# Performance work log

Hardware: AMD Instinct MI355X
Metric: run time of the kernel (lower is better)

Reference implementation:

```python
import jax, jax.numpy as jnp
import numpy as np

N = 100000
D = 64
H = 4 * D  # 256
E = 1000000


def setup_inputs() -> dict:
    key = jax.random.key(0)
    ks = jax.random.split(key, 9)
    return {
        "loc_feat": jax.random.normal(ks[0], (N, D), dtype=jnp.float32),
        "geo_src": jax.random.randint(ks[1], (E,), 0, N),
        "geo_dst": jax.random.randint(ks[2], (E,), 0, N),
        "trans_src": jax.random.randint(ks[3], (E,), 0, N),
        "trans_dst": jax.random.randint(ks[4], (E,), 0, N),
        "trans_w": jax.random.uniform(ks[5], (E,), dtype=jnp.float32),
        "W1": jax.random.normal(ks[6], (D, H), dtype=jnp.float32) * (1.0 / np.sqrt(D)),
        "b1": jax.random.normal(ks[7], (H,), dtype=jnp.float32) * 0.01,
        "W2": jax.random.normal(ks[8], (H, 1), dtype=jnp.float32) * (1.0 / np.sqrt(H)),
    }


def reference(loc_feat, geo_src, geo_dst, trans_src, trans_dst, trans_w, W1, b1, W2):
    n = loc_feat.shape[0]
    # etype 'geo': copy_u + mean  -> segment mean of src features at dst
    geo_sum = jax.ops.segment_sum(loc_feat[geo_src], geo_dst, num_segments=n)
    cnt = jax.ops.segment_sum(jnp.ones(geo_src.shape[0], loc_feat.dtype), geo_dst, num_segments=n)
    geo = jnp.where(cnt[:, None] > 0, geo_sum / jnp.maximum(cnt, 1.0)[:, None], 0.0)
    # etype 'trans': u_mul_e + sum -> weighted segment sum
    trans = jax.ops.segment_sum(loc_feat[trans_src] * trans_w[:, None], trans_dst, num_segments=n)
    # semantic attention fuse over the two relation views
    z = jnp.stack([geo, trans], axis=1)          # [N, 2, D]
    h = jnp.tanh(jnp.einsum('nkd,dh->nkh', z, W1) + b1)  # [N, 2, H]
    w = jnp.einsum('nkh,ho->nko', h, W2).mean(0)  # [2, 1] (mean over nodes)
    beta = jax.nn.softmax(w, axis=0)              # [2, 1]
    return (beta[None, :, :] * z).sum(1)          # [N, D]
```

## Files before the change

### kernel.cpp

```cpp
#include <hip/hip_runtime.h>
#include <hip/hip_bf16.h>

#define N_NODES 100000
#define DIM 64
#define HID 256
#define E_EDGES 1000000
#define TWO_N (2 * N_NODES)
#define MLP_ROWBLOCKS (TWO_N / 64)

#define TILE 60
#define NBINS 1667
#define CAP 800
#define EPB 4096
#define FILL_BLOCKS 245

#define NCH 8
#define KEYS (TILE * NCH)

#define PACKF_BLOCKS 782
#define PACKW1_BLOCKS 32
#define PREP_BLOCKS (2 * FILL_BLOCKS + PACKF_BLOCKS + PACKW1_BLOCKS)

typedef short short8 __attribute__((ext_vector_type(8)));
typedef float f32x4 __attribute__((ext_vector_type(4)));
typedef unsigned short us4 __attribute__((ext_vector_type(4)));
typedef unsigned short us8 __attribute__((ext_vector_type(8)));

__device__ __forceinline__ float tanh_fast(float x) {
    x = fminf(fmaxf(x, -15.0f), 15.0f);
    float e = __expf(2.0f * x);
    return (e - 1.0f) / (e + 1.0f);
}

__device__ __forceinline__ unsigned short f2bf(float x) {
    unsigned u = __float_as_uint(x);
    u = u + 0x7FFFu + ((u >> 16) & 1u);
    return (unsigned short)(u >> 16);
}

__device__ __forceinline__ float bf2f(unsigned short u) {
    return __uint_as_float(((unsigned)u) << 16);
}

__global__ void __launch_bounds__(512) prep_kernel(
        const int* __restrict__ gs, const int* __restrict__ gd,
        const int* __restrict__ ts, const int* __restrict__ td,
        const float* __restrict__ tw,
        int* __restrict__ gcount,
        int* __restrict__ gbin, int2* __restrict__ tbin,
        const float* __restrict__ feat, unsigned short* __restrict__ fb,
        const float* __restrict__ W1, unsigned short* __restrict__ W1p) {
    __shared__ int   hist[NBINS];
    __shared__ int   adjS[NBINS];
    __shared__ int   curS[NBINS];
    __shared__ int   pS[EPB];
    __shared__ float w2S[EPB];
    __shared__ unsigned short binS[EPB];
    __shared__ int   wsumS[8];
    __shared__ int   wpreS[8];

    int t = threadIdx.x;
    int blk = blockIdx.x;

    if (blk >= 2 * FILL_BLOCKS) {
        int pb = blk - 2 * FILL_BLOCKS;
        if (pb < PACKF_BLOCKS) {
            #pragma unroll
            for (int j = 0; j < 4; ++j) {
                int i = pb * 2048 + j * 512 + t;
                if (i < N_NODES * DIM / 4) {
                    float4 v = ((const float4*)feat)[i];
                    us4 o;
                    o[0] = f2bf(v.x); o[1] = f2bf(v.y); o[2] = f2bf(v.z); o[3] = f2bf(v.w);
                    ((us4*)fb)[i] = o;
                }
            }
        } else {
            int i = (pb - PACKF_BLOCKS) * 512 + t;
            int j = i & 7;
            int r = i >> 3;
            int nidx = r & 15; r >>= 4;
            int q = r & 3; r >>= 2;
            int khalf = r & 1;
            int n = r >> 1;
            int k = 32 * khalf + 8 * q + j;
            int c = 16 * n + nidx;
            W1p[i] = f2bf(W1[k * HID + c]);
        }
        return;
    }

    int lane = t & 63, wv = t >> 6;
    int rel = (blk >= FILL_BLOCKS) ? 1 : 0;
    int e0 = (rel ? blk - FILL_BLOCKS : blk) * EPB;
    const int* dstp = rel ? td : gd;
    const int* srcp = rel ? ts : gs;

    for (int i = t; i < NBINS; i += 512) hist[i] = 0;
    __syncthreads();

    int d_[8], s_[8];
    float w_[8];
    #pragma unroll
    for (int j = 0; j < 2; ++j) {
        int idx = e0 + j * 2048 + 4 * t;
        if (idx + 3 < E_EDGES) {
            int4 dv = *(const int4*)&dstp[idx];
            int4 sv = *(const int4*)&srcp[idx];
            d_[4*j+0] = dv.x; d_[4*j+1] = dv.y; d_[4*j+2] = dv.z; d_[4*j+3] = dv.w;
            s_[4*j+0] = sv.x; s_[4*j+1] = sv.y; s_[4*j+2] = sv.z; s_[4*j+3] = sv.w;
            if (rel) {
                float4 wvv = *(const float4*)&tw[idx];
                w_[4*j+0] = wvv.x; w_[4*j+1] = wvv.y; w_[4*j+2] = wvv.z; w_[4*j+3] = wvv.w;
            }
        } else {
            #pragma unroll
            for (int i2 = 0; i2 < 4; ++i2) {
                bool ok = (idx + i2 < E_EDGES);
                d_[4*j+i2] = ok ? dstp[idx + i2] : -1;
                s_[4*j+i2] = ok ? srcp[idx + i2] : 0;
                w_[4*j+i2] = (ok && rel) ? tw[idx + i2] : 0.0f;
            }
        }
    }
    #pragma unroll
    for (int i = 0; i < 8; ++i)
        if (d_[i] >= 0) atomicAdd(&hist[d_[i] / TILE], 1);
    __syncthreads();

    int carry = 0;
    for (int cb = 0; cb < NBINS; cb += 512) {
        int i = cb + t;
        int c = (i < NBINS) ? hist[i] : 0;
        int v = c;
        #pragma unroll
        for (int off = 1; off < 64; off <<= 1) {
            int u = __shfl_up(v, off);
            if (lane >= off) v += u;
        }
        if (lane == 63) wsumS[wv] = v;
        __syncthreads();
        if (t == 0) {
            int s = 0;
            #pragma unroll
            for (int w = 0; w < 8; ++w) { s += wsumS[w]; wpreS[w] = s; }
        }
        __syncthreads();
        int woff = (wv == 0) ? 0 : wpreS[wv - 1];
        if (i < NBINS) {
            int lb = carry + woff + v - c;
            curS[i] = lb;
            int gb = (c > 0) ? (i * CAP + atomicAdd(&gcount[rel * NBINS + i], c)) : 0;
            adjS[i] = gb - lb;
        }
        carry += wpreS[7];
        __syncthreads();
    }
    __syncthreads();

    #pragma unroll
    for (int i = 0; i < 8; ++i) {
        int d = d_[i];
        if (d < 0) continue;
        int bin = d / TILE;
        int pos = atomicAdd(&curS[bin], 1);
        pS[pos] = s_[i] | ((d - bin * TILE) << 20);
        binS[pos] = (unsigned short)bin;
        if (rel) w2S[pos] = w_[i];
    }
    __syncthreads();

    int nV = min(EPB, E_EDGES - e0);
    if (!rel) {
        for (int i = t; i < nV; i += 512) {
            int b = binS[i];
            int gi = adjS[b] + i;
            if (gi < (b + 1) * CAP)
                gbin[gi] = pS[i];
        }
    } else {
        for (int i = t; i < nV; i += 512) {
            int b = binS[i];
            int gi = adjS[b] + i;
            if (gi < (b + 1) * CAP)
                tbin[gi] = make_int2(pS[i], __float_as_int(w2S[i]));
        }
    }
}

__global__ void __launch_bounds__(256) aggregate_kernel(
        const unsigned short* __restrict__ featb,
        const int* __restrict__ gbin, const int2* __restrict__ tbin,
        const int* __restrict__ gcount,
        unsigned short* __restrict__ zb) {
    __shared__ int   srcS[CAP];
    __shared__ float wS[CAP];
    __shared__ int   histK[KEYS];
    __shared__ int   keyBase[KEYS];
    __shared__ int   keyCur[KEYS];
    __shared__ int   nodeB[TILE];
    __shared__ int   nodeD[TILE];
    __shared__ int   wsA[4];
    __shared__ int   wpA[4];

    int b = blockIdx.x;
    int rel = (b >= NBINS) ? 1 : 0;
    int bin = rel ? b - NBINS : b;
    int node0 = bin * TILE;
    int nNodes = min(TILE, N_NODES - node0);
    int t = threadIdx.x, lane = t & 63, wave = t >> 6;
    int oct = lane >> 3;
    int co = (lane & 7) * 8;

    int nE = gcount[b];
    if (nE > CAP) nE = CAP;

    for (int i = t; i < KEYS; i += 256) histK[i] = 0;
    __syncthreads();

    if (!rel) {
        const int* bp = gbin + (size_t)bin * CAP;
        for (int i = t; i < nE; i += 256) {
            int p = bp[i];
            int key = ((p >> 20) << 3) | ((p & 0xFFFFF) >> 14);
            atomicAdd(&histK[key], 1);
        }
    } else {
        const int2* bp = tbin + (size_t)bin * CAP;
        for (int i = t; i < nE; i += 256) {
            int p = bp[i].x;
            int key = ((p >> 20) << 3) | ((p & 0xFFFFF) >> 14);
            atomicAdd(&histK[key], 1);
        }
    }
    __syncthreads();

    int carry = 0;
    for (int cb = 0; cb < KEYS; cb += 256) {
        int i = cb + t;
        int c = (i < KEYS) ? histK[i] : 0;
        int v = c;
        #pragma unroll
        for (int off = 1; off < 64; off <<= 1) {
            int u = __shfl_up(v, off);
            if (lane >= off) v += u;
        }
        if (lane == 63) wsA[wave] = v;
        __syncthreads();
        if (t == 0) {
            int s = 0;
            #pragma unroll
            for (int w = 0; w < 4; ++w) { s += wsA[w]; wpA[w] = s; }
        }
        __syncthreads();
        int woff = (wave == 0) ? 0 : wpA[wave - 1];
        if (i < KEYS) {
            int lb = carry + woff + v - c;
            keyBase[i] = lb;
            keyCur[i] = lb;
        }
        carry += wpA[3];
        __syncthreads();
    }
    if (t < TILE) {
        int nb = keyBase[t * NCH];
        int nx = (t == TILE - 1) ? nE : keyBase[(t + 1) * NCH];
        nodeB[t] = nb;
        nodeD[t] = nx - nb;
    }
    __syncthreads();

    if (!rel) {
        const int* bp = gbin + (size_t)bin * CAP;
        for (int i = t; i < nE; i += 256) {
            int p = bp[i];
            int key = ((p >> 20) << 3) | ((p & 0xFFFFF) >> 14);
            int pos = atomicAdd(&keyCur[key], 1);
            srcS[pos] = p & 0xFFFFF;
        }
    } else {
        const int2* bp = tbin + (size_t)bin * CAP;
        for (int i = t; i < nE; i += 256) {
            int2 p = bp[i];
            int key = ((p.x >> 20) << 3) | ((p.x & 0xFFFFF) >> 14);
            int pos = atomicAdd(&keyCur[key], 1);
            srcS[pos] = p.x & 0xFFFFF;
            wS[pos] = __int_as_float(p.y);
        }
    }
    __syncthreads();

    for (int nl0 = wave * 8; nl0 < nNodes; nl0 += 32) {
        int nl = nl0 + oct;
        bool act = (nl < nNodes);
        int deg = act ? nodeD[nl] : 0;
        int base = act ? nodeB[nl] : 0;
        float a[8] = {0.f, 0.f, 0.f, 0.f, 0.f, 0.f, 0.f, 0.f};
        if (!rel) {
            int k = 0;
            for (; k + 3 < deg; k += 4) {
                int s0 = srcS[base + k],     s1 = srcS[base + k + 1];
                int s2 = srcS[base + k + 2], s3 = srcS[base + k + 3];
                us8 r0 = *(const us8*)&featb[(size_t)s0 * DIM + co];
                us8 r1 = *(const us8*)&featb[(size_t)s1 * DIM + co];
                us8 r2 = *(const us8*)&featb[(size_t)s2 * DIM + co];
                us8 r3 = *(const us8*)&featb[(size_t)s3 * DIM + co];
                #pragma unroll
                for (int j = 0; j < 8; ++j)
                    a[j] += (bf2f(r0[j]) + bf2f(r1[j])) + (bf2f(r2[j]) + bf2f(r3[j]));
            }
            for (; k < deg; ++k) {
                int s = srcS[base + k];
                us8 r = *(const us8*)&featb[(size_t)s * DIM + co];
                #pragma unroll
                for (int j = 0; j < 8; ++j) a[j] += bf2f(r[j]);
            }
        } else {
            int k = 0;
            for (; k + 3 < deg; k += 4) {
                int s0 = srcS[base + k],     s1 = srcS[base + k + 1];
                int s2 = srcS[base + k + 2], s3 = srcS[base + k + 3];
                float w0 = wS[base + k],     w1 = wS[base + k + 1];
                float w2 = wS[base + k + 2], w3 = wS[base + k + 3];
                us8 r0 = *(const us8*)&featb[(size_t)s0 * DIM + co];
                us8 r1 = *(const us8*)&featb[(size_t)s1 * DIM + co];
                us8 r2 = *(const us8*)&featb[(size_t)s2 * DIM + co];
                us8 r3 = *(const us8*)&featb[(size_t)s3 * DIM + co];
                #pragma unroll
                for (int j = 0; j < 8; ++j)
                    a[j] += (bf2f(r0[j]) * w0 + bf2f(r1[j]) * w1)
                          + (bf2f(r2[j]) * w2 + bf2f(r3[j]) * w3);
            }
            for (; k < deg; ++k) {
                int s = srcS[base + k];
                float w = wS[base + k];
                us8 r = *(const us8*)&featb[(size_t)s * DIM + co];
                #pragma unroll
                for (int j = 0; j < 8; ++j) a[j] += bf2f(r[j]) * w;
            }
        }
        if (act) {
            float sc = rel ? 1.0f : 1.0f / fmaxf((float)deg, 1.0f);
            us8 o;
            #pragma unroll
            for (int j = 0; j < 8; ++j) o[j] = f2bf(a[j] * sc);
            size_t row = (size_t)(rel ? N_NODES + node0 + nl : node0 + nl);
            *(us8*)&zb[row * DIM + co] = o;
        }
    }
}

__global__ void __launch_bounds__(256) mlp_mfma_kernel(
        const unsigned short* __restrict__ zb,
        const unsigned short* __restrict__ W1p,
        const float* __restrict__ bias1, const float* __restrict__ W2,
        float* __restrict__ partials) {
    __shared__ float wred[4][2];
    int t = threadIdx.x, lane = t & 63, wave = t >> 6;
    int m = lane & 15, q = lane >> 4;
    int base = blockIdx.x * 64 + wave * 16;
    int R = base + m;

    const unsigned short* rowp = zb + (size_t)R * DIM;
    short8 a0 = *(const short8*)(rowp + q * 8);
    short8 a1 = *(const short8*)(rowp + 32 + q * 8);

    float c0 = 0.0f, c1 = 0.0f;
    const short8* W1v = (const short8*)W1p;

    #pragma unroll 4
    for (int n = 0; n < 16; ++n) {
        short8 b0 = W1v[(n * 2 + 0) * 64 + lane];
        short8 bK = W1v[(n * 2 + 1) * 64 + lane];
        f32x4 acc = {0.0f, 0.0f, 0.0f, 0.0f};
        acc = __builtin_amdgcn_mfma_f32_16x16x32_bf16(a0, b0, acc, 0, 0, 0);
        acc = __builtin_amdgcn_mfma_f32_16x16x32_bf16(a1, bK, acc, 0, 0, 0);
        int col = 16 * n + m;
        float bj = bias1[col];
        float w2 = W2[col];
        #pragma unroll
        for (int reg = 0; reg < 4; ++reg) {
            int Rr = base + q * 4 + reg;
            float h = tanh_fast(acc[reg] + bj);
            float contrib = h * w2;
            if (Rr < N_NODES) c0 += contrib; else c1 += contrib;
        }
    }

    #pragma unroll
    for (int off = 32; off > 0; off >>= 1) {
        c0 += __shfl_down(c0, off);
        c1 += __shfl_down(c1, off);
    }
    if (lane == 0) { wred[wave][0] = c0; wred[wave][1] = c1; }
    __syncthreads();
    if (t == 0) {
        partials[blockIdx.x * 2 + 0] = wred[0][0] + wred[1][0] + wred[2][0] + wred[3][0];
        partials[blockIdx.x * 2 + 1] = wred[0][1] + wred[1][1] + wred[2][1] + wred[3][1];
    }
}

__global__ void __launch_bounds__(256) combine_kernel(
        const unsigned short* __restrict__ zb,
        const float* __restrict__ partials,
        float* __restrict__ out) {
    __shared__ float wred[4][2];
    __shared__ float bS[2];
    int t = threadIdx.x, lane = t & 63, wv = t >> 6;

    float c0 = 0.0f, c1 = 0.0f;
    for (int i = t; i < MLP_ROWBLOCKS; i += 256) {
        c0 += partials[i * 2 + 0];
        c1 += partials[i * 2 + 1];
    }
    #pragma unroll
    for (int off = 32; off > 0; off >>= 1) {
        c0 += __shfl_down(c0, off);
        c1 += __shfl_down(c1, off);
    }
    if (lane == 0) { wred[wv][0] = c0; wred[wv][1] = c1; }
    __syncthreads();
    if (t == 0) {
        float s0 = (wred[0][0] + wred[1][0] + wred[2][0] + wred[3][0]) / (float)N_NODES;
        float s1 = (wred[0][1] + wred[1][1] + wred[2][1] + wred[3][1]) / (float)N_NODES;
        float m = fmaxf(s0, s1);
        float e0 = __expf(s0 - m), e1 = __expf(s1 - m);
        float inv = 1.0f / (e0 + e1);
        bS[0] = e0 * inv;
        bS[1] = e1 * inv;
    }
    __syncthreads();
    float b0 = bS[0];
    float b1 = bS[1];

    int gid = blockIdx.x * 256 + t;
    uint4 g = *(const uint4*)&zb[(size_t)gid * 8];
    uint4 tr = *(const uint4*)&zb[(size_t)N_NODES * DIM + (size_t)gid * 8];
    float4 o0, o1;
    o0.x = b0 * __uint_as_float(g.x << 16) + b1 * __uint_as_float(tr.x << 16);
    o0.y = b0 * __uint_as_float(g.x & 0xFFFF0000u) + b1 * __uint_as_float(tr.x & 0xFFFF0000u);
    o0.z = b0 * __uint_as_float(g.y << 16) + b1 * __uint_as_float(tr.y << 16);
    o0.w = b0 * __uint_as_float(g.y & 0xFFFF0000u) + b1 * __uint_as_float(tr.y & 0xFFFF0000u);
    o1.x = b0 * __uint_as_float(g.z << 16) + b1 * __uint_as_float(tr.z << 16);
    o1.y = b0 * __uint_as_float(g.z & 0xFFFF0000u) + b1 * __uint_as_float(tr.z & 0xFFFF0000u);
    o1.z = b0 * __uint_as_float(g.w << 16) + b1 * __uint_as_float(tr.w << 16);
    o1.w = b0 * __uint_as_float(g.w & 0xFFFF0000u) + b1 * __uint_as_float(tr.w & 0xFFFF0000u);
    *(float4*)&out[(size_t)gid * 8] = o0;
    *(float4*)&out[(size_t)gid * 8 + 4] = o1;
}

extern "C" void kernel_launch(void* const* d_in, const int* in_sizes, int n_in,
                              void* d_out, int out_size, void* d_ws, size_t ws_size,
                              hipStream_t stream) {
    const float* loc_feat = (const float*)d_in[0];
    const int* geo_src    = (const int*)d_in[1];
    const int* geo_dst    = (const int*)d_in[2];
    const int* trans_src  = (const int*)d_in[3];
    const int* trans_dst  = (const int*)d_in[4];
    const float* trans_w  = (const float*)d_in[5];
    const float* W1       = (const float*)d_in[6];
    const float* b1       = (const float*)d_in[7];
    const float* W2       = (const float*)d_in[8];
    float* out = (float*)d_out;

    int*   gcount   = (int*)d_ws;
    int*   gbin     = gcount + 2 * NBINS;
    int2*  tbin     = (int2*)(gbin + (size_t)NBINS * CAP);
    float* partials = (float*)(tbin + (size_t)NBINS * CAP);
    float* beta     = partials + 2 * MLP_ROWBLOCKS;
    unsigned short* W1p   = (unsigned short*)(beta + 2);
    unsigned short* featb = W1p + 16384;
    unsigned short* zb    = featb + (size_t)N_NODES * DIM;

    hipMemsetAsync(gcount, 0, 2 * NBINS * sizeof(int), stream);

    prep_kernel<<<PREP_BLOCKS, 512, 0, stream>>>(geo_src, geo_dst, trans_src,
                                                 trans_dst, trans_w,
                                                 gcount, gbin, tbin,
                                                 loc_feat, featb, W1, W1p);
    aggregate_kernel<<<2 * NBINS, 256, 0, stream>>>(featb, gbin, tbin, gcount, zb);
    mlp_mfma_kernel<<<MLP_ROWBLOCKS, 256, 0, stream>>>(zb, W1p, b1, W2, partials);
    combine_kernel<<<(N_NODES * DIM / 8) / 256, 256, 0, stream>>>(zb, partials, out);
}
```

Baseline: 238.0 us.

## Merge geo and trans aggregation per node tile into one block with chunk-ordered gathers

Measured after the change: 233.5 us. Within noise of the previous version (-1.9%).

```diff
diff --git a/kernel.cpp b/kernel.cpp
--- a/kernel.cpp
+++ b/kernel.cpp
@@ -188,57 +188,13 @@
     }
 }
 
-__global__ void __launch_bounds__(256) aggregate_kernel(
-        const unsigned short* __restrict__ featb,
-        const int* __restrict__ gbin, const int2* __restrict__ tbin,
-        const int* __restrict__ gcount,
-        unsigned short* __restrict__ zb) {
-    __shared__ int   srcS[CAP];
-    __shared__ float wS[CAP];
-    __shared__ int   histK[KEYS];
-    __shared__ int   keyBase[KEYS];
-    __shared__ int   keyCur[KEYS];
-    __shared__ int   nodeB[TILE];
-    __shared__ int   nodeD[TILE];
-    __shared__ int   wsA[4];
-    __shared__ int   wpA[4];
-
-    int b = blockIdx.x;
-    int rel = (b >= NBINS) ? 1 : 0;
-    int bin = rel ? b - NBINS : b;
-    int node0 = bin * TILE;
-    int nNodes = min(TILE, N_NODES - node0);
-    int t = threadIdx.x, lane = t & 63, wave = t >> 6;
-    int oct = lane >> 3;
-    int co = (lane & 7) * 8;
-
-    int nE = gcount[b];
-    if (nE > CAP) nE = CAP;
-
-    for (int i = t; i < KEYS; i += 256) histK[i] = 0;
-    __syncthreads();
-
-    if (!rel) {
-        const int* bp = gbin + (size_t)bin * CAP;
-        for (int i = t; i < nE; i += 256) {
-            int p = bp[i];
-            int key = ((p >> 20) << 3) | ((p & 0xFFFFF) >> 14);
-            atomicAdd(&histK[key], 1);
-        }
-    } else {
-        const int2* bp = tbin + (size_t)bin * CAP;
-        for (int i = t; i < nE; i += 256) {
-            int p = bp[i].x;
-            int key = ((p >> 20) << 3) | ((p & 0xFFFFF) >> 14);
-            atomicAdd(&histK[key], 1);
-        }
-    }
-    __syncthreads();
-
+__device__ __forceinline__ void scan_keys(int* hist, int* kb, int* cur,
+                                          int* wsA, int* wpA, int nE,
+                                          int t, int lane, int wave) {
     int carry = 0;
     for (int cb = 0; cb < KEYS; cb += 256) {
         int i = cb + t;
-        int c = (i < KEYS) ? histK[i] : 0;
+        int c = (i < KEYS) ? hist[i] : 0;
         int v = c;
         #pragma unroll
         for (int off = 1; off < 64; off <<= 1) {
@@ -256,97 +212,137 @@
         int woff = (wave == 0) ? 0 : wpA[wave - 1];
         if (i < KEYS) {
             int lb = carry + woff + v - c;
-            keyBase[i] = lb;
-            keyCur[i] = lb;
+            kb[i] = lb;
+            cur[i] = lb;
         }
         carry += wpA[3];
         __syncthreads();
     }
-    if (t < TILE) {
-        int nb = keyBase[t * NCH];
-        int nx = (t == TILE - 1) ? nE : keyBase[(t + 1) * NCH];
-        nodeB[t] = nb;
-        nodeD[t] = nx - nb;
-    }
-    __syncthreads();
-
-    if (!rel) {
-        const int* bp = gbin + (size_t)bin * CAP;
-        for (int i = t; i < nE; i += 256) {
-            int p = bp[i];
-            int key = ((p >> 20) << 3) | ((p & 0xFFFFF) >> 14);
-            int pos = atomicAdd(&keyCur[key], 1);
-            srcS[pos] = p & 0xFFFFF;
-        }
-    } else {
-        const int2* bp = tbin + (size_t)bin * CAP;
-        for (int i = t; i < nE; i += 256) {
-            int2 p = bp[i];
-            int key = ((p.x >> 20) << 3) | ((p.x & 0xFFFFF) >> 14);
-            int pos = atomicAdd(&keyCur[key], 1);
-            srcS[pos] = p.x & 0xFFFFF;
-            wS[pos] = __int_as_float(p.y);
-        }
-    }
-    __syncthreads();
-
-    for (int nl0 = wave * 8; nl0 < nNodes; nl0 += 32) {
-        int nl = nl0 + oct;
-        bool act = (nl < nNodes);
-        int deg = act ? nodeD[nl] : 0;
-        int base = act ? nodeB[nl] : 0;
-        float a[8] = {0.f, 0.f, 0.f, 0.f, 0.f, 0.f, 0.f, 0.f};
-        if (!rel) {
-            int k = 0;
-            for (; k + 3 < deg; k += 4) {
-                int s0 = srcS[base + k],     s1 = srcS[base + k + 1];
-                int s2 = srcS[base + k + 2], s3 = srcS[base + k + 3];
-                us8 r0 = *(const us8*)&featb[(size_t)s0 * DIM + co];
-                us8 r1 = *(const us8*)&featb[(size_t)s1 * DIM + co];
-                us8 r2 = *(const us8*)&featb[(size_t)s2 * DIM + co];
-                us8 r3 = *(const us8*)&featb[(size_t)s3 * DIM + co];
+    if (t == 0) kb[KEYS] = nE;
+    __syncthreads();
+}
+
+__global__ void __launch_bounds__(256, 8) aggregate_kernel(
+        const unsigned short* __restrict__ featb,
+        const int* __restrict__ gbin, const int2* __restrict__ tbin,
+        const int* __restrict__ gcount,
+        unsigned short* __restrict__ zb) {
+    __shared__ int   srcG[CAP];
+    __shared__ int   srcT[CAP];
+    __shared__ float wT[CAP];
+    __shared__ int   kbG[KEYS + 1];
+    __shared__ int   kbT[KEYS + 1];
+    __shared__ int   histK[KEYS];
+    __shared__ int   curK[KEYS];
+    __shared__ int   wsA[4];
+    __shared__ int   wpA[4];
+
+    int bin = blockIdx.x;
+    int node0 = bin * TILE;
+    int nNodes = min(TILE, N_NODES - node0);
+    int t = threadIdx.x, lane = t & 63, wave = t >> 6;
+    int g = wave * 8 + (lane >> 3);
+    int co = (lane & 7) * 8;
+
+    int nEg = min(gcount[bin], CAP);
+    int nEt = min(gcount[NBINS + bin], CAP);
+    const int*  bpg = gbin + (size_t)bin * CAP;
+    const int2* bpt = tbin + (size_t)bin * CAP;
+
+    for (int i = t; i < KEYS; i += 256) histK[i] = 0;
+    __syncthreads();
+    for (int i = t; i < nEg; i += 256) {
+        int p = bpg[i];
+        atomicAdd(&histK[((p >> 20) << 3) | ((p & 0xFFFFF) >> 14)], 1);
+    }
+    __syncthreads();
+    scan_keys(histK, kbG, curK, wsA, wpA, nEg, t, lane, wave);
+    for (int i = t; i < nEg; i += 256) {
+        int p = bpg[i];
+        int key = ((p >> 20) << 3) | ((p & 0xFFFFF) >> 14);
+        int pos = atomicAdd(&curK[key], 1);
+        srcG[pos] = p & 0xFFFFF;
+    }
+    __syncthreads();
+
+    for (int i = t; i < KEYS; i += 256) histK[i] = 0;
+    __syncthreads();
+    for (int i = t; i < nEt; i += 256) {
+        int p = bpt[i].x;
+        atomicAdd(&histK[((p >> 20) << 3) | ((p & 0xFFFFF) >> 14)], 1);
+    }
+    __syncthreads();
+    scan_keys(histK, kbT, curK, wsA, wpA, nEt, t, lane, wave);
+    for (int i = t; i < nEt; i += 256) {
+        int2 p = bpt[i];
+        int key = ((p.x >> 20) << 3) | ((p.x & 0xFFFFF) >> 14);
+        int pos = atomicAdd(&curK[key], 1);
+        srcT[pos] = p.x & 0xFFFFF;
+        wT[pos]   = __int_as_float(p.y);
+    }
+    __syncthreads();
+
+    float aGA[8] = {0.f,0.f,0.f,0.f,0.f,0.f,0.f,0.f};
+    float aGB[8] = {0.f,0.f,0.f,0.f,0.f,0.f,0.f,0.f};
+    float aTA[8] = {0.f,0.f,0.f,0.f,0.f,0.f,0.f,0.f};
+    float aTB[8] = {0.f,0.f,0.f,0.f,0.f,0.f,0.f,0.f};
+    int nA = g, nB = g + 32;
+    bool hasB = (nB < TILE);
+
+    for (int c = 0; c < NCH; ++c) {
+        {
+            int s = kbG[nA * NCH + c], e = kbG[nA * NCH + c + 1];
+            for (int k = s; k < e; ++k) {
+                us8 r = *(const us8*)&featb[(size_t)srcG[k] * DIM + co];
                 #pragma unroll
-                for (int j = 0; j < 8; ++j)
-                    a[j] += (bf2f(r0[j]) + bf2f(r1[j])) + (bf2f(r2[j]) + bf2f(r3[j]));
-            }
-            for (; k < deg; ++k) {
-                int s = srcS[base + k];
-                us8 r = *(const us8*)&featb[(size_t)s * DIM + co];
+                for (int j = 0; j < 8; ++j) aGA[j] += bf2f(r[j]);
+            }
+        }
+        if (hasB) {
+            int s = kbG[nB * NCH + c], e = kbG[nB * NCH + c + 1];
+            for (int k = s; k < e; ++k) {
+                us8 r = *(const us8*)&featb[(size_t)srcG[k] * DIM + co];
                 #pragma unroll
-                for (int j = 0; j < 8; ++j) a[j] += bf2f(r[j]);
-            }
-        } else {
-            int k = 0;
-            for (; k + 3 < deg; k += 4) {
-                int s0 = srcS[base + k],     s1 = srcS[base + k + 1];
-                int s2 = srcS[base + k + 2], s3 = srcS[base + k + 3];
-                float w0 = wS[base + k],     w1 = wS[base + k + 1];
-                float w2 = wS[base + k + 2], w3 = wS[base + k + 3];
-                us8 r0 = *(const us8*)&featb[(size_t)s0 * DIM + co];
-                us8 r1 = *(const us8*)&featb[(size_t)s1 * DIM + co];
-                us8 r2 = *(const us8*)&featb[(size_t)s2 * DIM + co];
-                us8 r3 = *(const us8*)&featb[(size_t)s3 * DIM + co];
+                for (int j = 0; j < 8; ++j) aGB[j] += bf2f(r[j]);
+            }
+        }
+        {
+            int s = kbT[nA * NCH + c], e = kbT[nA * NCH + c + 1];
+            for (int k = s; k < e; ++k) {
+                float w = wT[k];
+                us8 r = *(const us8*)&featb[(size_t)srcT[k] * DIM + co];
                 #pragma unroll
-                for (int j = 0; j < 8; ++j)
-                    a[j] += (bf2f(r0[j]) * w0 + bf2f(r1[j]) * w1)
-                          + (bf2f(r2[j]) * w2 + bf2f(r3[j]) * w3);
-            }
-            for (; k < deg; ++k) {
-                int s = srcS[base + k];
-                float w = wS[base + k];
-                us8 r = *(const us8*)&featb[(size_t)s * DIM + co];
+                for (int j = 0; j < 8; ++j) aTA[j] += bf2f(r[j]) * w;
+            }
+        }
+        if (hasB) {
+            int s = kbT[nB * NCH + c], e = kbT[nB * NCH + c + 1];
+            for (int k = s; k < e; ++k) {
+                float w = wT[k];
+                us8 r = *(const us8*)&featb[(size_t)srcT[k] * DIM + co];
                 #pragma unroll
-                for (int j = 0; j < 8; ++j) a[j] += bf2f(r[j]) * w;
-            }
-        }
-        if (act) {
-            float sc = rel ? 1.0f : 1.0f / fmaxf((float)deg, 1.0f);
-            us8 o;
-            #pragma unroll
-            for (int j = 0; j < 8; ++j) o[j] = f2bf(a[j] * sc);
-            size_t row = (size_t)(rel ? N_NODES + node0 + nl : node0 + nl);
-            *(us8*)&zb[row * DIM + co] = o;
-        }
+                for (int j = 0; j < 8; ++j) aTB[j] += bf2f(r[j]) * w;
+            }
+        }
+    }
+
+    if (nA < nNodes) {
+        int degA = kbG[(nA + 1) * NCH] - kbG[nA * NCH];
+        float sc = 1.0f / fmaxf((float)degA, 1.0f);
+        us8 og, ot;
+        #pragma unroll
+        for (int j = 0; j < 8; ++j) { og[j] = f2bf(aGA[j] * sc); ot[j] = f2bf(aTA[j]); }
+        *(us8*)&zb[(size_t)(node0 + nA) * DIM + co] = og;
+        *(us8*)&zb[(size_t)(N_NODES + node0 + nA) * DIM + co] = ot;
+    }
+    if (hasB && nB < nNodes) {
+        int degB = kbG[(nB + 1) * NCH] - kbG[nB * NCH];
+        float sc = 1.0f / fmaxf((float)degB, 1.0f);
+        us8 og, ot;
+        #pragma unroll
+        for (int j = 0; j < 8; ++j) { og[j] = f2bf(aGB[j] * sc); ot[j] = f2bf(aTB[j]); }
+        *(us8*)&zb[(size_t)(node0 + nB) * DIM + co] = og;
+        *(us8*)&zb[(size_t)(N_NODES + node0 + nB) * DIM + co] = ot;
     }
 }
 
@@ -478,7 +474,7 @@
                                                  trans_dst, trans_w,
                                                  gcount, gbin, tbin,
                                                  loc_feat, featb, W1, W1p);
-    aggregate_kernel<<<2 * NBINS, 256, 0, stream>>>(featb, gbin, tbin, gcount, zb);
+    aggregate_kernel<<<NBINS, 256, 0, stream>>>(featb, gbin, tbin, gcount, zb);
     mlp_mfma_kernel<<<MLP_ROWBLOCKS, 256, 0, stream>>>(zb, W1p, b1, W2, partials);
     combine_kernel<<<(N_NODES * DIM / 8) / 256, 256, 0, stream>>>(zb, partials, out);
 }
```
